# Optimization experiments

Measured on AMD Instinct MI355X. Metric: run time of the kernel, lower is better.

## Reference

```python
import jax, jax.numpy as jnp
import numpy as np

B, T, D = 8, 2048, 1024   # batch, seq_len (== block_size), n_embed
HS = 128                   # head_size

def setup_inputs() -> dict:
    key = jax.random.key(0)
    kx, kk, kq, kv = jax.random.split(key, 4)
    s = D ** -0.5  # torch Linear default init scale ~ U(-1/sqrt(in), 1/sqrt(in))
    x  = jax.random.normal(kx, (B, T, D), dtype=jnp.float32)
    Wk = jax.random.uniform(kk, (HS, D), jnp.float32, -s, s)
    Wq = jax.random.uniform(kq, (HS, D), jnp.float32, -s, s)
    Wv = jax.random.uniform(kv, (HS, D), jnp.float32, -s, s)
    return {"x": x, "Wk": Wk, "Wq": Wq, "Wv": Wv}

def reference(x, Wk, Wq, Wv):
    # single-head causal self-attention; dropout disabled (eval mode)
    Tlen = x.shape[1]
    k = jnp.einsum('btd,hd->bth', x, Wk)   # [B,T,HS]
    q = jnp.einsum('btd,hd->bth', x, Wq)
    v = jnp.einsum('btd,hd->bth', x, Wv)
    scale = Wk.shape[0] ** -0.5
    scores = jnp.einsum('bth,bsh->bts', q, k) * scale   # [B,T,T]
    causal = jnp.tril(jnp.ones((Tlen, Tlen), dtype=bool))
    scores = jnp.where(causal, scores, -jnp.inf)
    weights = jax.nn.softmax(scores, axis=-1)
    out = jnp.einsum('bts,bsh->bth', weights, v)        # [B,T,HS]
    return out
```

## Files before the change

kernel.cpp:

```cpp
#include <hip/hip_runtime.h>
#include <hip/hip_bf16.h>
#include <math.h>

#define BATCH_N 8
#define SEQ_T   2048
#define DIM_D   1024
#define HS_N    128

using bf16x8_t = __attribute__((ext_vector_type(8))) __bf16;
using bf16x4_t = __attribute__((ext_vector_type(4))) __bf16;
using f32x4_t  = __attribute__((ext_vector_type(4))) float;

__device__ __forceinline__ f32x4_t mfma_16x16x32(bf16x8_t a, bf16x8_t b, f32x4_t c) {
  return __builtin_amdgcn_mfma_f32_16x16x32_bf16(a, b, c, 0, 0, 0);
}

__device__ __forceinline__ void async_cp16(const void* g, void* l) {
  __builtin_amdgcn_global_load_lds(
      (const __attribute__((address_space(1))) unsigned int*)g,
      (__attribute__((address_space(3))) unsigned int*)l, 16, 0, 0);
}

#define BAR()      __builtin_amdgcn_s_barrier()
#define FENCE()    asm volatile("" ::: "memory")
#define WAIT_VM(n) asm volatile("s_waitcnt vmcnt(" #n ")" ::: "memory")
#define WAIT_LGKM0 asm volatile("s_waitcnt lgkmcnt(0)" ::: "memory")

__global__ __launch_bounds__(256) void castw_kernel(
    const float* __restrict__ Wk, const float* __restrict__ Wq,
    const float* __restrict__ Wv, __bf16* __restrict__ Wb,
    unsigned int* __restrict__ km) {
  if (blockIdx.x == 0 && threadIdx.x < 8) km[threadIdx.x] = 0u;
  int idx = blockIdx.x * 256 + threadIdx.x;
  int e   = idx * 4;
  int row = e >> 10;
  int col = e & 1023;
  const float* src;
  float sc = 1.0f;
  if (row < 128) {
    src = Wk + row * DIM_D + col;
  } else if (row < 256) {
    src = Wq + (row - 128) * DIM_D + col;
    sc  = 0.08838834764831845f;
  } else {
    src = Wv + (row - 256) * DIM_D + col;
  }
  float4 v = *(const float4*)src;
  bf16x4_t o;
  o[0] = (__bf16)(v.x * sc); o[1] = (__bf16)(v.y * sc);
  o[2] = (__bf16)(v.z * sc); o[3] = (__bf16)(v.w * sc);
  *(bf16x4_t*)(Wb + e) = o;
}

__global__ __launch_bounds__(512, 2) void proj_kernel(
    const float* __restrict__ x, const __bf16* __restrict__ Wb,
    __bf16* __restrict__ Qb, __bf16* __restrict__ Kb, __bf16* __restrict__ Vt) {
  __shared__ __align__(16) char psmem[114688];
  __bf16* A = (__bf16*)psmem;

  const int tid  = threadIdx.x;
  const int lane = tid & 63;
  const int wave = tid >> 6;
  const int h    = wave >> 2;
  const int g    = wave & 3;
  const int lr = lane & 15;
  const int lq = lane >> 4;
  const int m0 = blockIdx.x * 64;

  f32x4_t acc[2][6];
  #pragma unroll
  for (int mt = 0; mt < 2; ++mt)
    #pragma unroll
    for (int nt = 0; nt < 6; ++nt) acc[mt][nt] = (f32x4_t){0.f, 0.f, 0.f, 0.f};

  auto stageB = [&](int bufi, int kt) {
    __bf16* Bs = (__bf16*)(psmem + 65536 + bufi * 24576);
    for (int c = wave; c < 24; c += 8) {
      const int row = c * 16 + (lane >> 2);
      const int u   = (lane & 3) ^ ((row >> 1) & 3);
      async_cp16(Wb + (size_t)row * DIM_D + kt * 32 + u * 8, Bs + c * 512);
    }
  };

  stageB(0, 0);

  for (int p = 0; p < 2; ++p) {
    __syncthreads();

    {
      const int r  = tid >> 3;
      const int t  = tid & 7;
      const float* xs = x + (size_t)(m0 + r) * DIM_D + p * 512;
      __bf16* as = A + r * 512;
      const int sw = r & 7;
      #pragma unroll
      for (int i = 0; i < 8; ++i) {
        const int u = t + 8 * i;
        float4 f0 = *(const float4*)(xs + u * 8);
        float4 f1 = *(const float4*)(xs + u * 8 + 4);
        bf16x8_t a;
        a[0] = (__bf16)f0.x; a[1] = (__bf16)f0.y;
        a[2] = (__bf16)f0.z; a[3] = (__bf16)f0.w;
        a[4] = (__bf16)f1.x; a[5] = (__bf16)f1.y;
        a[6] = (__bf16)f1.z; a[7] = (__bf16)f1.w;
        *(bf16x8_t*)(as + ((u ^ sw) * 8)) = a;
      }
    }
    __syncthreads();

    for (int kt2 = 0; kt2 < 16; ++kt2) {
      const int kt  = p * 16 + kt2;
      const int cur = kt & 1;
      if (kt + 1 < 32) {
        stageB(cur ^ 1, kt + 1);
        WAIT_VM(3);
      } else {
        WAIT_VM(0);
      }
      BAR();
      FENCE();
      const __bf16* Bs = (const __bf16*)(psmem + 65536 + cur * 24576);

      bf16x8_t af[2];
      #pragma unroll
      for (int mt = 0; mt < 2; ++mt) {
        const int ml = h * 32 + mt * 16 + lr;
        const int u  = kt2 * 4 + lq;
        af[mt] = *(const bf16x8_t*)(&A[ml * 512 + ((u ^ (ml & 7)) * 8)]);
      }
      bf16x8_t bfv[6];
      #pragma unroll
      for (int nt = 0; nt < 6; ++nt) {
        const int nl = g * 96 + nt * 16 + lr;
        bfv[nt] = *(const bf16x8_t*)(&Bs[nl * 32 + ((lq ^ ((nl >> 1) & 3)) * 8)]);
      }
      #pragma unroll
      for (int mt = 0; mt < 2; ++mt)
        #pragma unroll
        for (int nt = 0; nt < 6; ++nt)
          acc[mt][nt] = mfma_16x16x32(af[mt], bfv[nt], acc[mt][nt]);
      WAIT_LGKM0;
      BAR();
      FENCE();
    }
  }

  #pragma unroll
  for (int mt = 0; mt < 2; ++mt) {
    const int t0 = m0 + h * 32 + mt * 16 + lq * 4;
    #pragma unroll
    for (int nt = 0; nt < 6; ++nt) {
      const int nn = g * 96 + nt * 16 + lr;
      if (nn < 256) {
        __bf16* dst = (nn < 128) ? (Kb + nn) : (Qb + (nn - 128));
        #pragma unroll
        for (int r = 0; r < 4; ++r)
          dst[(size_t)(t0 + r) * HS_N] = (__bf16)acc[mt][nt][r];
      } else {
        const int bb = t0 >> 11;
        const int tl = t0 & 2047;
        bf16x4_t o;
        #pragma unroll
        for (int r = 0; r < 4; ++r) o[r] = (__bf16)acc[mt][nt][r];
        *(bf16x4_t*)(Vt + (size_t)bb * (HS_N * SEQ_T) + (size_t)(nn - 256) * SEQ_T + tl) = o;
      }
    }
  }
}

__global__ __launch_bounds__(256) void knorm_kernel(
    const __bf16* __restrict__ Kb, unsigned int* __restrict__ km) {
  const int t = blockIdx.x * 256 + threadIdx.x;
  const __bf16* kp = Kb + (size_t)t * HS_N;
  float ss = 0.f;
  #pragma unroll
  for (int i = 0; i < 16; ++i) {
    bf16x8_t v = *(const bf16x8_t*)(kp + i * 8);
    #pragma unroll
    for (int j = 0; j < 8; ++j) { float f = (float)v[j]; ss += f * f; }
  }
  #pragma unroll
  for (int off = 1; off < 64; off <<= 1) ss = fmaxf(ss, __shfl_xor(ss, off));
  if ((threadIdx.x & 63) == 0) atomicMax(km + (t >> 11), __float_as_uint(ss));
}

__global__ __launch_bounds__(256, 2) void attn_kernel(
    const __bf16* __restrict__ Qb, const __bf16* __restrict__ Kb,
    const __bf16* __restrict__ Vt, const unsigned int* __restrict__ km,
    __bf16* __restrict__ Opart, float* __restrict__ lpart) {
  __shared__ __align__(16) char smem[81920];
  __bf16* KsBase = (__bf16*)smem;
  __bf16* VsBase = (__bf16*)(smem + 32768);
  float*  Ofl    = (float*)smem;

  const int lane = threadIdx.x & 63;
  const int wave = threadIdx.x >> 6;
  const int lr = lane & 15;
  const int lq = lane >> 4;
  const int bid  = blockIdx.x;
  const int b    = bid & 7;
  const int rest = bid >> 3;
  const int jg   = 15 - (rest >> 2);
  const int p4   = rest & 3;
  const int Q0   = jg * 128;
  const int qa   = Q0 + wave * 32;
  const int ch   = 2 * (jg + 1);
  const int c0   = (p4 * ch) >> 2;
  const int c1   = ((p4 + 1) * ch) >> 2;

  const __bf16* Qbb = Qb + (size_t)b * (SEQ_T * HS_N);
  const __bf16* Kbb = Kb + (size_t)b * (SEQ_T * HS_N);
  const __bf16* Vbb = Vt + (size_t)b * (HS_N * SEQ_T);
  __bf16* pbA = (__bf16*)(smem + 65536 + wave * 4096);
  __bf16* pbB = (__bf16*)(smem + 65536 + wave * 4096 + 2048);

  bf16x8_t qf[2][4];
  #pragma unroll
  for (int t = 0; t < 2; ++t)
    #pragma unroll
    for (int ks = 0; ks < 4; ++ks)
      qf[t][ks] = *(const bf16x8_t*)(Qbb + (size_t)(qa + t * 16 + lr) * HS_N
                                     + ks * 32 + lq * 8);

  const float km2 = __uint_as_float(km[b]);
  float mrow[2][4];
  #pragma unroll
  for (int t = 0; t < 2; ++t) {
    float qn2 = 0.f;
    #pragma unroll
    for (int ks = 0; ks < 4; ++ks)
      #pragma unroll
      for (int j = 0; j < 8; ++j) { float f = (float)qf[t][ks][j]; qn2 += f * f; }
    qn2 += __shfl_xor(qn2, 16);
    qn2 += __shfl_xor(qn2, 32);
    #pragma unroll
    for (int r2 = 0; r2 < 4; ++r2)
      mrow[t][r2] = sqrtf(__shfl(qn2, lq * 4 + r2) * km2);
  }

  f32x4_t Oa[2][8];
  #pragma unroll
  for (int t = 0; t < 2; ++t)
    #pragma unroll
    for (int o = 0; o < 8; ++o) Oa[t][o] = (f32x4_t){0.f, 0.f, 0.f, 0.f};
  float lsum[2][4] = {{0.f,0.f,0.f,0.f},{0.f,0.f,0.f,0.f}};

  auto stage = [&](int bufi, int c) {
    const int kk = c * 64;
    __bf16* Ks = KsBase + bufi * 8192;
    for (int idx = wave; idx < 32; idx += 4) {
      if (idx < 16) {
        const int row = idx * 4 + (lane >> 4);
        const int u   = (lane & 15) ^ (row & 15);
        async_cp16(Kbb + (size_t)(kk + row) * HS_N + u * 8, Ks + idx * 512);
      } else {
        const int i2  = idx - 16;
        const int row = i2 * 8 + (lane >> 3);
        const int u   = (lane & 7) ^ (row & 7);
        async_cp16(Vbb + (size_t)row * SEQ_T + kk + u * 8, VsBase + bufi * 8192 + i2 * 512);
      }
    }
  };

  if (c0 < c1) stage(0, c0);
  __syncthreads();

  for (int c = c0; c < c1; ++c) {
    const int cur = (c - c0) & 1;
    if (c + 1 < c1) {
      stage(cur ^ 1, c + 1);
      WAIT_VM(8);
    } else {
      WAIT_VM(0);
    }
    BAR();
    FENCE();

    const int kk = c * 64;
    const __bf16* Ks = KsBase + cur * 8192;
    const __bf16* Vs = VsBase + cur * 8192;

    f32x4_t s0[4], s1[4];
    #pragma unroll
    for (int nt = 0; nt < 4; ++nt) {
      s0[nt] = (f32x4_t){0.f, 0.f, 0.f, 0.f};
      s1[nt] = (f32x4_t){0.f, 0.f, 0.f, 0.f};
    }
    #pragma unroll
    for (int ks = 0; ks < 4; ++ks)
      #pragma unroll
      for (int nt = 0; nt < 4; ++nt) {
        bf16x8_t kf = *(const bf16x8_t*)(
            &Ks[(nt * 16 + lr) * 128 + (((ks * 4 + lq) ^ lr) * 8)]);
        s0[nt] = mfma_16x16x32(qf[0][ks], kf, s0[nt]);
        s1[nt] = mfma_16x16x32(qf[1][ks], kf, s1[nt]);
      }
    const int q0a = qa, q0b = qa + 16;
    if (kk + 63 > q0a) {
      #pragma unroll
      for (int nt = 0; nt < 4; ++nt) {
        const int col = kk + nt * 16 + lr;
        #pragma unroll
        for (int r2 = 0; r2 < 4; ++r2)
          if (col > q0a + lq * 4 + r2) s0[nt][r2] = -INFINITY;
      }
    }
    if (kk + 63 > q0b) {
      #pragma unroll
      for (int nt = 0; nt < 4; ++nt) {
        const int col = kk + nt * 16 + lr;
        #pragma unroll
        for (int r2 = 0; r2 < 4; ++r2)
          if (col > q0b + lq * 4 + r2) s1[nt][r2] = -INFINITY;
      }
    }

    #pragma unroll
    for (int r2 = 0; r2 < 4; ++r2) {
      float a0 = __expf(s0[0][r2] - mrow[0][r2]);
      float a1 = __expf(s0[1][r2] - mrow[0][r2]);
      float a2 = __expf(s0[2][r2] - mrow[0][r2]);
      float a3 = __expf(s0[3][r2] - mrow[0][r2]);
      s0[0][r2] = a0; s0[1][r2] = a1; s0[2][r2] = a2; s0[3][r2] = a3;
      lsum[0][r2] += (a0 + a1) + (a2 + a3);
      float b0 = __expf(s1[0][r2] - mrow[1][r2]);
      float b1 = __expf(s1[1][r2] - mrow[1][r2]);
      float b2 = __expf(s1[2][r2] - mrow[1][r2]);
      float b3 = __expf(s1[3][r2] - mrow[1][r2]);
      s1[0][r2] = b0; s1[1][r2] = b1; s1[2][r2] = b2; s1[3][r2] = b3;
      lsum[1][r2] += (b0 + b1) + (b2 + b3);
    }

    #pragma unroll
    for (int nt = 0; nt < 4; ++nt)
      #pragma unroll
      for (int r2 = 0; r2 < 4; ++r2) {
        const int prow = lq * 4 + r2;
        const int pcol = (nt * 16 + lr) ^ ((prow & 7) << 3);
        pbA[prow * 64 + pcol] = (__bf16)s0[nt][r2];
        pbB[prow * 64 + pcol] = (__bf16)s1[nt][r2];
      }

    #pragma unroll
    for (int k2 = 0; k2 < 2; ++k2) {
      const int au = ((k2 * 4 + lq) ^ (lr & 7)) << 3;
      bf16x8_t afrA = *(const bf16x8_t*)(pbA + lr * 64 + au);
      bf16x8_t afrB = *(const bf16x8_t*)(pbB + lr * 64 + au);
      #pragma unroll
      for (int o = 0; o < 8; ++o) {
        bf16x8_t vfr = *(const bf16x8_t*)(
            &Vs[(o * 16 + lr) * 64 + (((k2 * 4 + lq) ^ (lr & 7)) * 8)]);
        Oa[0][o] = mfma_16x16x32(afrA, vfr, Oa[0][o]);
        Oa[1][o] = mfma_16x16x32(afrB, vfr, Oa[1][o]);
      }
    }
    WAIT_LGKM0;
    BAR();
    FENCE();
  }

  #pragma unroll
  for (int t = 0; t < 2; ++t)
    #pragma unroll
    for (int r2 = 0; r2 < 4; ++r2) {
      float v = lsum[t][r2];
      v += __shfl_xor(v, 1);
      v += __shfl_xor(v, 2);
      v += __shfl_xor(v, 4);
      v += __shfl_xor(v, 8);
      if (lr == 0)
        lpart[bid * 128 + wave * 32 + t * 16 + lq * 4 + r2] = v;
    }

  #pragma unroll
  for (int t = 0; t < 2; ++t)
    #pragma unroll
    for (int o = 0; o < 8; ++o)
      #pragma unroll
      for (int r2 = 0; r2 < 4; ++r2)
        Ofl[(wave * 32 + t * 16 + lq * 4 + r2) * 132 + o * 16 + lr] = Oa[t][o][r2];
  __syncthreads();

  {
    const int row = threadIdx.x >> 1;
    const int cb  = (threadIdx.x & 1) * 64;
    __bf16* dst = Opart + ((size_t)bid * 128 + row) * 128 + cb;
    #pragma unroll
    for (int g2 = 0; g2 < 16; ++g2) {
      float4 f = *(const float4*)(&Ofl[row * 132 + cb + g2 * 4]);
      bf16x4_t o;
      o[0] = (__bf16)f.x; o[1] = (__bf16)f.y; o[2] = (__bf16)f.z; o[3] = (__bf16)f.w;
      *(bf16x4_t*)(dst + g2 * 4) = o;
    }
  }
}

__global__ __launch_bounds__(256) void merge_kernel(
    const __bf16* __restrict__ Opart, const float* __restrict__ lpart,
    float* __restrict__ out) {
  const int idx = blockIdx.x * 256 + threadIdx.x;
  const int row = idx >> 5;
  const int c4  = (idx & 31) * 4;
  const int b   = row >> 11;
  const int tl  = row & 2047;
  const int jg  = tl >> 7;
  const int lrow = tl & 127;
  const int rbase = (15 - jg) * 4;
  float a0 = 0.f, a1 = 0.f, a2 = 0.f, a3 = 0.f, l = 0.f;
  #pragma unroll
  for (int p = 0; p < 4; ++p) {
    const int s = b + 8 * (rbase + p);
    bf16x4_t a = *(const bf16x4_t*)(Opart + ((size_t)s * 128 + lrow) * 128 + c4);
    a0 += (float)a[0]; a1 += (float)a[1]; a2 += (float)a[2]; a3 += (float)a[3];
    l += lpart[s * 128 + lrow];
  }
  const float inv = 1.0f / l;
  float4 o;
  o.x = a0 * inv; o.y = a1 * inv; o.z = a2 * inv; o.w = a3 * inv;
  *(float4*)(out + (size_t)row * HS_N + c4) = o;
}

extern "C" void kernel_launch(void* const* d_in, const int* in_sizes, int n_in,
                              void* d_out, int out_size, void* d_ws, size_t ws_size,
                              hipStream_t stream) {
  const float* x  = (const float*)d_in[0];
  const float* Wk = (const float*)d_in[1];
  const float* Wq = (const float*)d_in[2];
  const float* Wv = (const float*)d_in[3];
  float* out = (float*)d_out;

  char* ws = (char*)d_ws;
  __bf16* Wb = (__bf16*)ws;
  __bf16* Qb = (__bf16*)(ws + 786432);
  __bf16* Kb = (__bf16*)(ws + 786432 + 4194304);
  __bf16* Vt = (__bf16*)(ws + 786432 + 8388608);
  unsigned int* km = (unsigned int*)(ws + 13369344);
  __bf16* Opart = (__bf16*)(ws + 13369600);
  float*  lpart = (float*)(ws + 30146816);

  castw_kernel<<<384, 256, 0, stream>>>(Wk, Wq, Wv, Wb, km);
  proj_kernel<<<256, 512, 0, stream>>>(x, Wb, Qb, Kb, Vt);
  knorm_kernel<<<64, 256, 0, stream>>>(Kb, km);
  attn_kernel<<<512, 256, 0, stream>>>(Qb, Kb, Vt, km, Opart, lpart);
  merge_kernel<<<2048, 256, 0, stream>>>(Opart, lpart, out);
}
```

Before: 156.6 us.

## Fuse key-norm into projection and merge into attention; triple-buffer weights

The K-norm reduction now runs inside the projection epilogue from fp32 accumulators, and the split-K merge runs in the last-finishing attention block of each group via an atomic counter. This removes two kernel launches and the extra global reads of Kb and Opart. The projection weight staging moves from double to triple buffering, which raises LDS use and drops occupancy to one block per CU. The attention MFMA sections are also wrapped in s_setprio. The risks are lower projection occupancy and the merge now being serialized at the tail of the attention kernel.

```diff
diff --git a/kernel.cpp b/kernel.cpp
--- a/kernel.cpp
+++ b/kernel.cpp
@@ -29,8 +29,11 @@
 __global__ __launch_bounds__(256) void castw_kernel(
     const float* __restrict__ Wk, const float* __restrict__ Wq,
     const float* __restrict__ Wv, __bf16* __restrict__ Wb,
-    unsigned int* __restrict__ km) {
-  if (blockIdx.x == 0 && threadIdx.x < 8) km[threadIdx.x] = 0u;
+    unsigned int* __restrict__ km, unsigned int* __restrict__ cnt) {
+  if (blockIdx.x == 0) {
+    if (threadIdx.x < 8) km[threadIdx.x] = 0u;
+    if (threadIdx.x < 128) cnt[threadIdx.x] = 0u;
+  }
   int idx = blockIdx.x * 256 + threadIdx.x;
   int e   = idx * 4;
   int row = e >> 10;
@@ -52,10 +55,11 @@
   *(bf16x4_t*)(Wb + e) = o;
 }
 
-__global__ __launch_bounds__(512, 2) void proj_kernel(
+__global__ __launch_bounds__(512, 1) void proj_kernel(
     const float* __restrict__ x, const __bf16* __restrict__ Wb,
-    __bf16* __restrict__ Qb, __bf16* __restrict__ Kb, __bf16* __restrict__ Vt) {
-  __shared__ __align__(16) char psmem[114688];
+    __bf16* __restrict__ Qb, __bf16* __restrict__ Kb, __bf16* __restrict__ Vt,
+    unsigned int* __restrict__ km) {
+  __shared__ __align__(16) char psmem[139264];
   __bf16* A = (__bf16*)psmem;
 
   const int tid  = threadIdx.x;
@@ -73,8 +77,8 @@
     #pragma unroll
     for (int nt = 0; nt < 6; ++nt) acc[mt][nt] = (f32x4_t){0.f, 0.f, 0.f, 0.f};
 
-  auto stageB = [&](int bufi, int kt) {
-    __bf16* Bs = (__bf16*)(psmem + 65536 + bufi * 24576);
+  auto stageB = [&](int kt) {
+    __bf16* Bs = (__bf16*)(psmem + 65536 + (kt % 3) * 24576);
     for (int c = wave; c < 24; c += 8) {
       const int row = c * 16 + (lane >> 2);
       const int u   = (lane & 3) ^ ((row >> 1) & 3);
@@ -82,7 +86,8 @@
     }
   };
 
-  stageB(0, 0);
+  stageB(0);
+  stageB(1);
 
   for (int p = 0; p < 2; ++p) {
     __syncthreads();
@@ -109,17 +114,14 @@
     __syncthreads();
 
     for (int kt2 = 0; kt2 < 16; ++kt2) {
-      const int kt  = p * 16 + kt2;
-      const int cur = kt & 1;
-      if (kt + 1 < 32) {
-        stageB(cur ^ 1, kt + 1);
-        WAIT_VM(3);
-      } else {
-        WAIT_VM(0);
-      }
+      const int kt = p * 16 + kt2;
+      if (kt + 2 < 32) stageB(kt + 2);
+      if (kt < 30)       { WAIT_VM(6); }
+      else if (kt == 30) { WAIT_VM(3); }
+      else               { WAIT_VM(0); }
       BAR();
       FENCE();
-      const __bf16* Bs = (const __bf16*)(psmem + 65536 + cur * 24576);
+      const __bf16* Bs = (const __bf16*)(psmem + 65536 + (kt % 3) * 24576);
 
       bf16x8_t af[2];
       #pragma unroll
@@ -143,6 +145,32 @@
       BAR();
       FENCE();
     }
+  }
+
+  __syncthreads();
+  float* rowss = (float*)psmem;
+  if (tid < 64) rowss[tid] = 0.f;
+  __syncthreads();
+  if (g < 2) {
+    #pragma unroll
+    for (int mt = 0; mt < 2; ++mt)
+      #pragma unroll
+      for (int r = 0; r < 4; ++r) {
+        float s = 0.f;
+        #pragma unroll
+        for (int nt = 0; nt < 6; ++nt)
+          if (g == 0 || nt < 2) s += acc[mt][nt][r] * acc[mt][nt][r];
+        s += __shfl_xor(s, 1); s += __shfl_xor(s, 2);
+        s += __shfl_xor(s, 4); s += __shfl_xor(s, 8);
+        if (lr == 0) atomicAdd(&rowss[h * 32 + mt * 16 + lq * 4 + r], s);
+      }
+  }
+  __syncthreads();
+  if (tid < 64) {
+    float v = rowss[tid];
+    #pragma unroll
+    for (int off = 1; off < 64; off <<= 1) v = fmaxf(v, __shfl_xor(v, off));
+    if (tid == 0) atomicMax(km + (m0 >> 11), __float_as_uint(v));
   }
 
   #pragma unroll
@@ -168,26 +196,11 @@
   }
 }
 
-__global__ __launch_bounds__(256) void knorm_kernel(
-    const __bf16* __restrict__ Kb, unsigned int* __restrict__ km) {
-  const int t = blockIdx.x * 256 + threadIdx.x;
-  const __bf16* kp = Kb + (size_t)t * HS_N;
-  float ss = 0.f;
-  #pragma unroll
-  for (int i = 0; i < 16; ++i) {
-    bf16x8_t v = *(const bf16x8_t*)(kp + i * 8);
-    #pragma unroll
-    for (int j = 0; j < 8; ++j) { float f = (float)v[j]; ss += f * f; }
-  }
-  #pragma unroll
-  for (int off = 1; off < 64; off <<= 1) ss = fmaxf(ss, __shfl_xor(ss, off));
-  if ((threadIdx.x & 63) == 0) atomicMax(km + (t >> 11), __float_as_uint(ss));
-}
-
 __global__ __launch_bounds__(256, 2) void attn_kernel(
     const __bf16* __restrict__ Qb, const __bf16* __restrict__ Kb,
     const __bf16* __restrict__ Vt, const unsigned int* __restrict__ km,
-    __bf16* __restrict__ Opart, float* __restrict__ lpart) {
+    __bf16* __restrict__ Opart, float* __restrict__ lpart,
+    unsigned int* __restrict__ cnt, float* __restrict__ out) {
   __shared__ __align__(16) char smem[81920];
   __bf16* KsBase = (__bf16*)smem;
   __bf16* VsBase = (__bf16*)(smem + 32768);
@@ -286,6 +299,7 @@
       s0[nt] = (f32x4_t){0.f, 0.f, 0.f, 0.f};
       s1[nt] = (f32x4_t){0.f, 0.f, 0.f, 0.f};
     }
+    __builtin_amdgcn_s_setprio(1);
     #pragma unroll
     for (int ks = 0; ks < 4; ++ks)
       #pragma unroll
@@ -295,6 +309,7 @@
         s0[nt] = mfma_16x16x32(qf[0][ks], kf, s0[nt]);
         s1[nt] = mfma_16x16x32(qf[1][ks], kf, s1[nt]);
       }
+    __builtin_amdgcn_s_setprio(0);
     const int q0a = qa, q0b = qa + 16;
     if (kk + 63 > q0a) {
       #pragma unroll
@@ -346,6 +361,7 @@
       const int au = ((k2 * 4 + lq) ^ (lr & 7)) << 3;
       bf16x8_t afrA = *(const bf16x8_t*)(pbA + lr * 64 + au);
       bf16x8_t afrB = *(const bf16x8_t*)(pbB + lr * 64 + au);
+      __builtin_amdgcn_s_setprio(1);
       #pragma unroll
       for (int o = 0; o < 8; ++o) {
         bf16x8_t vfr = *(const bf16x8_t*)(
@@ -353,6 +369,7 @@
         Oa[0][o] = mfma_16x16x32(afrA, vfr, Oa[0][o]);
         Oa[1][o] = mfma_16x16x32(afrB, vfr, Oa[1][o]);
       }
+      __builtin_amdgcn_s_setprio(0);
     }
     WAIT_LGKM0;
     BAR();
@@ -393,31 +410,45 @@
       *(bf16x4_t*)(dst + g2 * 4) = o;
     }
   }
-}
-
-__global__ __launch_bounds__(256) void merge_kernel(
-    const __bf16* __restrict__ Opart, const float* __restrict__ lpart,
-    float* __restrict__ out) {
-  const int idx = blockIdx.x * 256 + threadIdx.x;
-  const int row = idx >> 5;
-  const int c4  = (idx & 31) * 4;
-  const int b   = row >> 11;
-  const int tl  = row & 2047;
-  const int jg  = tl >> 7;
-  const int lrow = tl & 127;
-  const int rbase = (15 - jg) * 4;
-  float a0 = 0.f, a1 = 0.f, a2 = 0.f, a3 = 0.f, l = 0.f;
-  #pragma unroll
-  for (int p = 0; p < 4; ++p) {
-    const int s = b + 8 * (rbase + p);
-    bf16x4_t a = *(const bf16x4_t*)(Opart + ((size_t)s * 128 + lrow) * 128 + c4);
-    a0 += (float)a[0]; a1 += (float)a[1]; a2 += (float)a[2]; a3 += (float)a[3];
-    l += lpart[s * 128 + lrow];
-  }
-  const float inv = 1.0f / l;
-  float4 o;
-  o.x = a0 * inv; o.y = a1 * inv; o.z = a2 * inv; o.w = a3 * inv;
-  *(float4*)(out + (size_t)row * HS_N + c4) = o;
+
+  __threadfence();
+  __syncthreads();
+  unsigned int* flagp = (unsigned int*)smem;
+  if (threadIdx.x == 0) {
+    const int gidx = (rest >> 2) * 8 + b;
+    unsigned int old = atomicAdd(&cnt[gidx], 1u);
+    flagp[0] = (old == 3u) ? 1u : 0u;
+  }
+  __syncthreads();
+  if (flagp[0] != 0u) {
+    __threadfence();
+    const int row = threadIdx.x >> 1;
+    const int cb  = (threadIdx.x & 1) * 64;
+    const int rbase = (rest >> 2) * 4;
+    int s[4];
+    float l = 0.f;
+    #pragma unroll
+    for (int p2 = 0; p2 < 4; ++p2) {
+      s[p2] = b + 8 * (rbase + p2);
+      l += lpart[s[p2] * 128 + row];
+    }
+    const float inv = 1.0f / l;
+    float* dst = out + ((size_t)b * SEQ_T + (size_t)jg * 128 + row) * HS_N + cb;
+    #pragma unroll
+    for (int g2 = 0; g2 < 16; ++g2) {
+      float o0 = 0.f, o1 = 0.f, o2 = 0.f, o3 = 0.f;
+      #pragma unroll
+      for (int p2 = 0; p2 < 4; ++p2) {
+        bf16x4_t a = *(const bf16x4_t*)(
+            Opart + ((size_t)s[p2] * 128 + row) * 128 + cb + g2 * 4);
+        o0 += (float)a[0]; o1 += (float)a[1];
+        o2 += (float)a[2]; o3 += (float)a[3];
+      }
+      float4 o;
+      o.x = o0 * inv; o.y = o1 * inv; o.z = o2 * inv; o.w = o3 * inv;
+      *(float4*)(dst + g2 * 4) = o;
+    }
+  }
 }
 
 extern "C" void kernel_launch(void* const* d_in, const int* in_sizes, int n_in,
@@ -434,13 +465,12 @@
   __bf16* Qb = (__bf16*)(ws + 786432);
   __bf16* Kb = (__bf16*)(ws + 786432 + 4194304);
   __bf16* Vt = (__bf16*)(ws + 786432 + 8388608);
-  unsigned int* km = (unsigned int*)(ws + 13369344);
-  __bf16* Opart = (__bf16*)(ws + 13369600);
-  float*  lpart = (float*)(ws + 30146816);
-
-  castw_kernel<<<384, 256, 0, stream>>>(Wk, Wq, Wv, Wb, km);
-  proj_kernel<<<256, 512, 0, stream>>>(x, Wb, Qb, Kb, Vt);
-  knorm_kernel<<<64, 256, 0, stream>>>(Kb, km);
-  attn_kernel<<<512, 256, 0, stream>>>(Qb, Kb, Vt, km, Opart, lpart);
-  merge_kernel<<<2048, 256, 0, stream>>>(Opart, lpart, out);
-}
+  unsigned int* km  = (unsigned int*)(ws + 13369344);
+  unsigned int* cnt = (unsigned int*)(ws + 13369408);
+  __bf16* Opart = (__bf16*)(ws + 13370368);
+  float*  lpart = (float*)(ws + 30147584);
+
+  castw_kernel<<<384, 256, 0, stream>>>(Wk, Wq, Wv, Wb, km, cnt);
+  proj_kernel<<<256, 512, 0, stream>>>(x, Wb, Qb, Kb, Vt, km);
+  attn_kernel<<<512, 256, 0, stream>>>(Qb, Kb, Vt, km, Opart, lpart, cnt, out);
+}
```

Result: slower. 249.6 us (+59.4%).
